# Optimization experiments

Hardware: AMD Instinct MI355X
Metric: run time of the kernel (lower is better)

## Reference

```python
import jax, jax.numpy as jnp
import numpy as np

N_NODES, N_GRAPHS, N_EDGES = 40960, 1024, 163840


def setup_inputs() -> dict:
    key = jax.random.key(0)
    ks = jax.random.split(key, 40)
    w = lambda k, s: jax.random.normal(k, s, jnp.float32) * 0.05
    inp = {
        "x": jax.random.normal(ks[0], (N_NODES, 78), jnp.float32),
        "edge_index": jax.random.randint(ks[1], (2, N_EDGES), 0, N_NODES, jnp.int32),
        "batch": jnp.repeat(jnp.arange(N_GRAPHS, dtype=jnp.int32), N_NODES // N_GRAPHS),
        "target1": jax.random.normal(ks[2], (N_GRAPHS, 750, 20), jnp.float32),
        "target2": jax.random.randint(ks[3], (N_GRAPHS, 750), 0, 26, jnp.int32),
        # GCN layers
        "W1": w(ks[4], (78, 78)), "b1": jnp.zeros((78,), jnp.float32),
        "W2": w(ks[5], (78, 156)), "b2": jnp.zeros((156,), jnp.float32),
        "W3": w(ks[6], (156, 312)), "b3": jnp.zeros((312,), jnp.float32),
        "Wg1": w(ks[7], (312, 1024)), "bg1": jnp.zeros((1024,), jnp.float32),
        "Wg2": w(ks[8], (1024, 128)), "bg2": jnp.zeros((128,), jnp.float32),
        # protein branch
        "emb": w(ks[9], (26, 128)),
        "Wc2": w(ks[10], (32, 750, 8)), "bc2": jnp.zeros((32,), jnp.float32),
        "Wxt2": w(ks[11], (32 * 121, 128)), "bxt2": jnp.zeros((128,), jnp.float32),
        "Wc1": w(ks[12], (32, 750, 8)), "bc1": jnp.zeros((32,), jnp.float32),
        "Wxt1": w(ks[13], (416, 128)), "bxt1": jnp.zeros((128,), jnp.float32),
        # fusion head
        "Wf1": w(ks[14], (384, 1024)), "bf1": jnp.zeros((1024,), jnp.float32),
        "Wf2": w(ks[15], (1024, 512)), "bf2": jnp.zeros((512,), jnp.float32),
        "Wo": w(ks[16], (512, 1)), "bo": jnp.zeros((1,), jnp.float32),
    }
    return inp


def _conv1d(x, w, b):
    # x: [B, C_in, L], w: [C_out, C_in, K] -> [B, C_out, L-K+1]
    y = jax.lax.conv_general_dilated(x, w, (1,), "VALID",
                                     dimension_numbers=("NCH", "OIH", "NCH"))
    return y + b[None, :, None]


def reference(x, edge_index, batch, target1, target2,
              W1, b1, W2, b2, W3, b3, Wg1, bg1, Wg2, bg2,
              emb, Wc2, bc2, Wxt2, bxt2, Wc1, bc1, Wxt1, bxt1,
              Wf1, bf1, Wf2, bf2, Wo, bo):
    N = x.shape[0]
    loop = jnp.arange(N, dtype=edge_index.dtype)
    src = jnp.concatenate([edge_index[0], loop])  # message source j
    dst = jnp.concatenate([edge_index[1], loop])  # aggregation target i
    # symmetric GCN normalization with self-loops (degree from dst, as in PyG)
    deg = jnp.zeros((N,), x.dtype).at[dst].add(1.0)
    dinv = jax.lax.rsqrt(deg)  # deg >= 1 due to self loops
    norm = (dinv[src] * dinv[dst])[:, None]

    def gcn(h, W, b):
        m = (h @ W)[src] * norm
        return jax.ops.segment_sum(m, dst, num_segments=N) + b

    h = jax.nn.relu(gcn(x, W1, b1))
    h = jax.nn.relu(gcn(h, W2, b2))
    h = jax.nn.relu(gcn(h, W3, b3))
    # global max pool per graph
    g = jax.ops.segment_max(h, batch, num_segments=N_GRAPHS)
    g = jax.nn.relu(g @ Wg1 + bg1)
    g = g @ Wg2 + bg2  # dropout is identity at inference

    # protein branch 2: embedding -> conv1d over channels=750
    e = emb[target2]                         # [B, 750, 128]
    xt2 = _conv1d(e, Wc2, bc2)               # [B, 32, 121]
    xt2 = xt2.reshape(-1, 32 * 121) @ Wxt2 + bxt2

    # protein branch 1: raw float features
    xt1 = _conv1d(target1, Wc1, bc1)         # [B, 32, 13]
    xt1 = xt1.reshape(-1, 416) @ Wxt1 + bxt1

    xc = jnp.concatenate([g, xt1, xt2], axis=1)  # [B, 384]
    xc = jax.nn.relu(xc @ Wf1 + bf1)
    xc = jax.nn.relu(xc @ Wf2 + bf2)
    return xc @ Wo + bo
```

## Files before the change

### kernel.cpp

```cpp
#include <hip/hip_runtime.h>
#include <hip/hip_bf16.h>

#define NN 40960
#define NE 163840
#define NB 1024

typedef __attribute__((ext_vector_type(8))) short short8;
typedef __attribute__((ext_vector_type(4))) short short4v;
typedef __attribute__((ext_vector_type(4))) float floatx4;

__device__ inline unsigned short f2bf(float f) {
    union { float f; unsigned u; } v; v.f = f;
    unsigned r = v.u + 0x7fffu + ((v.u >> 16) & 1u);
    return (unsigned short)(r >> 16);
}
__device__ inline float bf2f(unsigned short s) {
    union { unsigned u; float f; } v; v.u = ((unsigned)s) << 16; return v.f;
}
__device__ inline unsigned pack2bf(float lo, float hi) {
    return (unsigned)f2bf(lo) | ((unsigned)f2bf(hi) << 16);
}

static const size_t o_dinv = 0, o_g312 = 40960, o_g1024 = 360448, o_xc = 1409024,
                    o_f1 = 1802240, o_f2 = 2850816, o_b1v = 3375104, o_b2v = 3375232,
                    o_iws = 3375360, o_bufA = 3621124, o_bufB = 16400644;

__global__ __launch_bounds__(256) void k_histprep(
    const int* __restrict__ dst, int* __restrict__ cnt, int* __restrict__ flag,
    const float* __restrict__ W1, const float* __restrict__ W2, const float* __restrict__ W3,
    const float* __restrict__ Wg1, const float* __restrict__ Wg2, const float* __restrict__ Wf1,
    const float* __restrict__ Wf2, unsigned short* __restrict__ Wt,
    const float* __restrict__ Wc2, const float* __restrict__ Wc1,
    float* __restrict__ Wc2r, float* __restrict__ Wc1r,
    const float* __restrict__ Wxt1, float* __restrict__ Btb,
    const float* __restrict__ bc1, const float* __restrict__ bxt1, float* __restrict__ b1v,
    const float* __restrict__ bc2, const float* __restrict__ Wxt2, const float* __restrict__ bxt2,
    float* __restrict__ b2v,
    const float* __restrict__ emb, float* __restrict__ T) {
    __shared__ float el[128];
    int bx = blockIdx.x, tid = threadIdx.x;
    if (bx < 640) {
        int e = bx * 256 + tid;
        if (e < NE) atomicAdd(&cnt[dst[e]], 1);
        return;
    }
    int bp = bx - 640;
    if (bp == 0 && tid == 0) *flag = 0;
    if (bp < 3328) {
        const int cum[8]  = {0, 128, 320, 640, 1664, 1792, 2816, 3328};
        const int KP[7]   = {96, 96, 160, 320, 1024, 384, 1024};
        const int KB[7]   = {78, 78, 156, 312, 1024, 384, 1024};
        const int NNm[7]  = {78, 156, 312, 1024, 128, 1024, 512};
        const size_t OFF[7] = {0, 12288, 30720, 81920, 409600, 540672, 933888};
        int m = 0;
        while (m < 6 && bp >= cum[m + 1]) m++;
        int r = bp - cum[m];
        const float* src = (m == 0) ? W1 : (m == 1) ? W2 : (m == 2) ? W3 : (m == 3) ? Wg1
                         : (m == 4) ? Wg2 : (m == 5) ? Wf1 : Wf2;
        int kp = KP[m], kb = KB[m], nn = NNm[m];
        unsigned short* d = Wt + OFF[m] + (size_t)r * kp;
        for (int k = tid; k < kp; k += 256) {
            float v = (r < nn && k < kb) ? src[(size_t)k * nn + r] : 0.f;
            d[k] = f2bf(v);
        }
    } else if (bp < 4828) {
        int cc = bp - 3328, j = tid;
        const float* W = (cc < 750) ? Wc2 : Wc1;
        float* Wr = (cc < 750) ? Wc2r : Wc1r;
        int c = (cc < 750) ? cc : cc - 750;
        Wr[(size_t)c * 256 + j] = W[(size_t)(j >> 3) * 6000 + c * 8 + (j & 7)];
    } else if (bp < 7388) {
        int idx = (bp - 4828) * 256 + tid;
        int j = idx & 127, ok = (idx >> 7) & 255, t = idx >> 15;
        int o = ok >> 3, k = ok & 7, lpos = t - k;
        float v = (lpos >= 0 && lpos < 13) ? Wxt1[(size_t)(o * 13 + lpos) * 128 + j] : 0.f;
        Btb[(size_t)(t * 256 + ok) * 128 + j] = v;
    } else if (bp < 7452) {
        if (tid >= 128) return;
        int b = bp - 7388, j = tid;
        if (b < 32) {
            const float* p = Wxt1 + (size_t)b * 13 * 128 + j;
            float t = 0.f;
            for (int l = 0; l < 13; l++) t += p[(size_t)l * 128];
            float add = bc1[b] * t + ((b == 0) ? bxt1[j] : 0.f);
            atomicAdd(&b1v[j], add);
        } else {
            int o = b - 32;
            const float* p = Wxt2 + (size_t)o * 121 * 128 + j;
            float t = 0.f;
            for (int l = 0; l < 121; l++) t += p[(size_t)l * 128];
            float add = bc2[o] * t + ((o == 0) ? bxt2[j] : 0.f);
            atomicAdd(&b2v[j], add);
        }
    } else {
        int tb = bp - 7452;
        int v = tb >> 4, op = tb & 15;
        int o = op * 2 + (tid >> 7), j = tid & 127;
        if (tid < 128) el[j] = emb[(size_t)v * 128 + j];
        __syncthreads();
        float acc[8] = {};
        for (int l = 0; l < 121; l++) {
            float w = Wxt2[(size_t)(o * 121 + l) * 128 + j];
#pragma unroll
            for (int k = 0; k < 8; k++) acc[k] += el[l + k] * w;
        }
#pragma unroll
        for (int k = 0; k < 8; k++) T[(size_t)(v * 256 + o * 8 + k) * 128 + j] = acc[k];
    }
}

__global__ __launch_bounds__(1024) void k_scan_all(const int* __restrict__ cnt, int* __restrict__ off,
                                                   int* __restrict__ cur, float* __restrict__ dinv,
                                                   int* __restrict__ blockSum, int* __restrict__ flag) {
    __shared__ int lds[1024];
    __shared__ int bs[40];
    int tid = threadIdx.x, bx = blockIdx.x;
    int i = bx * 1024 + tid;
    int v = cnt[i];
    dinv[i] = rsqrtf((float)v + 1.0f);
    lds[tid] = v;
    __syncthreads();
    for (int s = 1; s < 1024; s <<= 1) {
        int t = (tid >= s) ? lds[tid - s] : 0;
        __syncthreads();
        lds[tid] += t;
        __syncthreads();
    }
    int localExcl = lds[tid] - v;
    if (tid == 1023) {
        atomicExch(&blockSum[bx], lds[1023]);
        __threadfence();
        atomicAdd(flag, 1);
    }
    if (tid == 0) {
        while (atomicAdd(flag, 0) < 40) { }
    }
    __syncthreads();
    if (tid < 40) bs[tid] = atomicAdd(&blockSum[tid], 0);
    __syncthreads();
    int pref = 0;
    for (int j = 0; j < bx; j++) pref += bs[j];
    int o = localExcl + pref;
    off[i] = o;
    cur[i] = o;
    if (i == NN - 1) off[NN] = NE;
}

__global__ __launch_bounds__(64) void k_agg_x(const float* __restrict__ x, const float* __restrict__ dinv,
                                              const int* __restrict__ off, const int* __restrict__ srcs,
                                              unsigned* __restrict__ out) {
    int n = blockIdx.x;
    int f = threadIdx.x;
    if (f >= 48) return;
    if (f >= 39) { out[(size_t)n * 48 + f] = 0; return; }
    float di = dinv[n];
    float2 sv = *(const float2*)&x[(size_t)n * 78 + 2 * f];
    float a0 = sv.x * di * di, a1 = sv.y * di * di;
    int e0 = off[n], e1 = off[n + 1];
    int e = e0;
    for (; e + 4 <= e1; e += 4) {
        int s0 = srcs[e], s1 = srcs[e + 1], s2 = srcs[e + 2], s3 = srcs[e + 3];
        float d0 = dinv[s0] * di, d1 = dinv[s1] * di, d2 = dinv[s2] * di, d3 = dinv[s3] * di;
        float2 v0 = *(const float2*)&x[(size_t)s0 * 78 + 2 * f];
        float2 v1 = *(const float2*)&x[(size_t)s1 * 78 + 2 * f];
        float2 v2 = *(const float2*)&x[(size_t)s2 * 78 + 2 * f];
        float2 v3 = *(const float2*)&x[(size_t)s3 * 78 + 2 * f];
        a0 += v0.x * d0 + v1.x * d1 + v2.x * d2 + v3.x * d3;
        a1 += v0.y * d0 + v1.y * d1 + v2.y * d2 + v3.y * d3;
    }
    for (; e < e1; e++) {
        int s = srcs[e];
        float dd = dinv[s] * di;
        float2 v = *(const float2*)&x[(size_t)s * 78 + 2 * f];
        a0 += v.x * dd; a1 += v.y * dd;
    }
    out[(size_t)n * 48 + f] = pack2bf(a0, a1);
}

__device__ inline void d_agg16_node(int n, int f, const unsigned* __restrict__ h,
                                    const float* __restrict__ dinv, const int* __restrict__ off,
                                    const int* __restrict__ srcs, unsigned* __restrict__ out, int F2) {
    if (f >= F2) return;
    float di = dinv[n];
    unsigned s0v = h[(size_t)n * F2 + f];
    float a0 = bf2f((unsigned short)(s0v & 0xffff)) * di * di;
    float a1 = bf2f((unsigned short)(s0v >> 16)) * di * di;
    int e0 = off[n], e1 = off[n + 1];
    int e = e0;
    for (; e + 4 <= e1; e += 4) {
        int s0 = srcs[e], s1 = srcs[e + 1], s2 = srcs[e + 2], s3 = srcs[e + 3];
        float d0 = dinv[s0] * di, d1 = dinv[s1] * di, d2 = dinv[s2] * di, d3 = dinv[s3] * di;
        unsigned v0 = h[(size_t)s0 * F2 + f];
        unsigned v1 = h[(size_t)s1 * F2 + f];
        unsigned v2 = h[(size_t)s2 * F2 + f];
        unsigned v3 = h[(size_t)s3 * F2 + f];
        a0 += bf2f((unsigned short)(v0 & 0xffff)) * d0 + bf2f((unsigned short)(v1 & 0xffff)) * d1
            + bf2f((unsigned short)(v2 & 0xffff)) * d2 + bf2f((unsigned short)(v3 & 0xffff)) * d3;
        a1 += bf2f((unsigned short)(v0 >> 16)) * d0 + bf2f((unsigned short)(v1 >> 16)) * d1
            + bf2f((unsigned short)(v2 >> 16)) * d2 + bf2f((unsigned short)(v3 >> 16)) * d3;
    }
    for (; e < e1; e++) {
        int s = srcs[e];
        float dd = dinv[s] * di;
        unsigned v = h[(size_t)s * F2 + f];
        a0 += bf2f((unsigned short)(v & 0xffff)) * dd;
        a1 += bf2f((unsigned short)(v >> 16)) * dd;
    }
    out[(size_t)n * F2 + f] = pack2bf(a0, a1);
}

__global__ void k_agg16(const unsigned* __restrict__ h, const float* __restrict__ dinv,
                        const int* __restrict__ off, const int* __restrict__ srcs,
                        unsigned* __restrict__ out, int F2) {
    d_agg16_node(blockIdx.x, threadIdx.x, h, dinv, off, srcs, out, F2);
}

#define LDST 72
template <bool ABF16, bool OUTBF16, bool ATOMIC, bool RELU_OUT>
__global__ __launch_bounds__(256) void gemm_bt(const void* __restrict__ Av, const unsigned short* __restrict__ Bt,
                                               const float* __restrict__ bias, void* __restrict__ Cv,
                                               int Nn, int Npad, int Kpad, int Klim,
                                               int lda, int ldb, int ldc, int ksplit) {
    __shared__ __align__(16) unsigned short As[64 * LDST];
    __shared__ __align__(16) unsigned short Bs[64 * LDST];
    const float* Af = (const float*)Av;
    const unsigned short* A16 = (const unsigned short*)Av;
    float* Cf = (float*)Cv;
    unsigned short* C16 = (unsigned short*)Cv;
    int bn0 = blockIdx.x * 64;
    int bm0 = blockIdx.y * 64;
    int k0 = blockIdx.z * ksplit;
    int kend = k0 + ksplit; if (kend > Kpad) kend = Kpad;
    int tid = threadIdx.x;
    int w = tid >> 6, l = tid & 63, q = l >> 4, r = l & 15;
    int wr = w >> 1, wc = w & 1;

    floatx4 acc[2][2];
#pragma unroll
    for (int i = 0; i < 2; i++)
#pragma unroll
        for (int c = 0; c < 2; c++) acc[i][c] = (floatx4)0.0f;

    int mA = tid >> 2, kcA = (tid & 3) * 8;
    int nB = tid >> 2, kcB = (tid & 3) * 8;
    int gmA = bm0 + mA;
    int gnB = bn0 + nB;

    for (int kt = k0; kt < kend; kt += 32) {
        if (ABF16) {
            *(short8*)&As[mA * LDST + kcA] = *(const short8*)(A16 + (size_t)gmA * lda + kt + kcA);
        } else {
            const float* Ap = Af + (size_t)gmA * lda + kt + kcA;
            float av[8];
            if (kt + kcA + 8 <= Klim) {
#pragma unroll
                for (int j = 0; j < 4; j++) {
                    float2 p = *(const float2*)(Ap + j * 2);
                    av[j * 2] = p.x; av[j * 2 + 1] = p.y;
                }
            } else {
#pragma unroll
                for (int j = 0; j < 8; j++) av[j] = (kt + kcA + j < Klim) ? Ap[j] : 0.f;
            }
            short8 sv;
#pragma unroll
            for (int j = 0; j < 8; j++) sv[j] = (short)f2bf(av[j]);
            *(short8*)&As[mA * LDST + kcA] = sv;
        }
        *(short8*)&Bs[nB * LDST + kcB] = *(const short8*)(Bt + (size_t)gnB * ldb + kt + kcB);
        __syncthreads();
        short8 a0 = *(const short8*)&As[(wr * 32 + r) * LDST + q * 8];
        short8 a1 = *(const short8*)&As[(wr * 32 + 16 + r) * LDST + q * 8];
        short8 b0 = *(const short8*)&Bs[(wc * 32 + r) * LDST + q * 8];
        short8 b1 = *(const short8*)&Bs[(wc * 32 + 16 + r) * LDST + q * 8];
        acc[0][0] = __builtin_amdgcn_mfma_f32_16x16x32_bf16(a0, b0, acc[0][0], 0, 0, 0);
        acc[0][1] = __builtin_amdgcn_mfma_f32_16x16x32_bf16(a0, b1, acc[0][1], 0, 0, 0);
        acc[1][0] = __builtin_amdgcn_mfma_f32_16x16x32_bf16(a1, b0, acc[1][0], 0, 0, 0);
        acc[1][1] = __builtin_amdgcn_mfma_f32_16x16x32_bf16(a1, b1, acc[1][1], 0, 0, 0);
        __syncthreads();
    }

#pragma unroll
    for (int c2 = 0; c2 < 2; c2++) {
        int col = bn0 + wc * 32 + c2 * 16 + r;
        if (col >= Npad) continue;
        bool live = col < Nn;
        float bv = (bias && live) ? bias[col] : 0.f;
#pragma unroll
        for (int i = 0; i < 2; i++) {
#pragma unroll
            for (int v = 0; v < 4; v++) {
                int row = bm0 + wr * 32 + i * 16 + q * 4 + v;
                float val = live ? (acc[i][c2][v] + bv) : 0.f;
                if (RELU_OUT) val = fmaxf(val, 0.f);
                if (OUTBF16) {
                    C16[(size_t)row * ldc + col] = live ? f2bf(val) : (unsigned short)0;
                } else if (live) {
                    if (ATOMIC) atomicAdd(&Cf[(size_t)row * ldc + col], val);
                    else Cf[(size_t)row * ldc + col] = val;
                }
            }
        }
    }
}

__global__ __launch_bounds__(256) void k_fbi(
    const int* __restrict__ ei, int* __restrict__ cur, int* __restrict__ srcOut,
    const float* __restrict__ Wc2r, const float* __restrict__ T,
    const float* __restrict__ Wc1r, const float* __restrict__ Btb,
    unsigned short* __restrict__ U16, unsigned short* __restrict__ Vt16,
    float* __restrict__ xc, float* __restrict__ f2,
    const float* __restrict__ bg2, const float* __restrict__ b1v, const float* __restrict__ bf2) {
    __shared__ __align__(16) unsigned short As[64 * LDST];
    __shared__ __align__(16) unsigned short Bs[64 * LDST];
    int bx = blockIdx.x, tid = threadIdx.x;
    if (bx < 640) {
        int e = bx * 256 + tid;
        if (e >= NE) return;
        int s = ei[e], d = ei[NE + e];
        int pos = atomicAdd(&cur[d], 1);
        srcOut[pos] = s;
        return;
    }
    if (bx >= 1744) {
        int b = bx - 1744;
        for (int t = tid; t < 768; t += 256) {
            if (t < 128) xc[(size_t)b * 384 + t] = bg2[t];
            else if (t < 256) xc[(size_t)b * 384 + t] = b1v[t - 128];
            else f2[(size_t)b * 512 + t - 256] = bf2[t - 256];
        }
        return;
    }
    int v = bx - 640;
    int gx = v & 1, gy = (v >> 1) % 12, gz = (v >> 1) / 12;
    const int M = 750, Nn = 128, K = 256;
    bool om1 = gz < 26;
    const float* A = om1 ? Wc2r : Wc1r;
    const float* Bm = om1 ? (T + (size_t)gz * 32768) : (Btb + (size_t)(gz - 26) * 32768);
    unsigned short* C16 = om1 ? (U16 + (size_t)gz * 128) : Vt16;
    int ldc = om1 ? 3328 : 15360;
    int zz = gz - 26;
    int bn0 = gx * 64;
    int bm0 = gy * 64;
    int w = tid >> 6, l = tid & 63, q = l >> 4, r = l & 15;
    int wr = w >> 1, wc = w & 1;

    floatx4 acc[2][2];
#pragma unroll
    for (int i = 0; i < 2; i++)
#pragma unroll
        for (int c = 0; c < 2; c++) acc[i][c] = (floatx4)0.0f;

    int mA = tid >> 2, kcA = (tid & 3) * 8;
    int nB = tid >> 2, kcB = (tid & 3) * 8;
    int gmA = bm0 + mA;
    int gnB = bn0 + nB;

    for (int kt = 0; kt < K; kt += 32) {
        {
            float av[8];
            const float* Ap = A + (size_t)gmA * K + kt + kcA;
            if (gmA < M) {
#pragma unroll
                for (int j = 0; j < 4; j++) {
                    float2 p = *(const float2*)(Ap + j * 2);
                    av[j * 2] = p.x; av[j * 2 + 1] = p.y;
                }
            } else {
#pragma unroll
                for (int j = 0; j < 8; j++) av[j] = 0.f;
            }
            short8 sv;
#pragma unroll
            for (int j = 0; j < 8; j++) sv[j] = (short)f2bf(av[j]);
            *(short8*)&As[mA * LDST + kcA] = sv;
        }
        {
            short8 sv;
#pragma unroll
            for (int j = 0; j < 8; j++) {
                int gk = kt + kcB + j;
                float vv = (gnB < Nn) ? Bm[(size_t)gk * Nn + gnB] : 0.f;
                sv[j] = (short)f2bf(vv);
            }
            *(short8*)&Bs[nB * LDST + kcB] = sv;
        }
        __syncthreads();
        short8 a0 = *(const short8*)&As[(wr * 32 + r) * LDST + q * 8];
        short8 a1 = *(const short8*)&As[(wr * 32 + 16 + r) * LDST + q * 8];
        short8 b0 = *(const short8*)&Bs[(wc * 32 + r) * LDST + q * 8];
        short8 b1 = *(const short8*)&Bs[(wc * 32 + 16 + r) * LDST + q * 8];
        acc[0][0] = __builtin_amdgcn_mfma_f32_16x16x32_bf16(a0, b0, acc[0][0], 0, 0, 0);
        acc[0][1] = __builtin_amdgcn_mfma_f32_16x16x32_bf16(a0, b1, acc[0][1], 0, 0, 0);
        acc[1][0] = __builtin_amdgcn_mfma_f32_16x16x32_bf16(a1, b0, acc[1][0], 0, 0, 0);
        acc[1][1] = __builtin_amdgcn_mfma_f32_16x16x32_bf16(a1, b1, acc[1][1], 0, 0, 0);
        __syncthreads();
    }

#pragma unroll
    for (int c = 0; c < 2; c++) {
        int col = bn0 + wc * 32 + c * 16 + r;
        if (col >= Nn) continue;
#pragma unroll
        for (int i = 0; i < 2; i++) {
#pragma unroll
            for (int vv = 0; vv < 4; vv++) {
                int row = bm0 + wr * 32 + i * 16 + q * 4 + vv;
                if (row >= M) continue;
                if (om1) C16[(size_t)row * ldc + col] = f2bf(acc[i][c][vv]);
                else C16[(size_t)col * ldc + row * 20 + zz] = f2bf(acc[i][c][vv]);
            }
        }
    }
}

#define T1LD 40
#define T1S  48
#define T1K  320
__global__ __launch_bounds__(256) void k_t1_l1(
    const float* __restrict__ t1A, const unsigned short* __restrict__ Bt, float* __restrict__ P,
    const unsigned short* __restrict__ A16, const unsigned short* __restrict__ W1t,
    const float* __restrict__ bias, unsigned short* __restrict__ C16) {
    __shared__ __align__(16) unsigned char smem[30720];
    int bx = blockIdx.x, tid = threadIdx.x;
    if (bx < 768) {
        unsigned short* AsS = (unsigned short*)smem;
        unsigned short* BsS = (unsigned short*)smem + 5120;
        const int Klim = 15000;
        int mt = bx & 15, ks = bx >> 4;
        int bm0 = mt * 64;
        int k0 = ks * T1K;
        int w = tid >> 6, l = tid & 63, q = l >> 4, r = l & 15;
        int wr = w >> 1, wc = w & 1;

        floatx4 acc[2][4];
#pragma unroll
        for (int i = 0; i < 2; i++)
#pragma unroll
            for (int c = 0; c < 4; c++) acc[i][c] = (floatx4)0.0f;

        int ra = tid >> 3, ca = (tid & 7) * 4;
        int rb = tid >> 2, cb = (tid & 3) * 8;
        const float* Ap0 = t1A + (size_t)(bm0 + ra) * Klim + ca;
        const float* Ap1 = t1A + (size_t)(bm0 + ra + 32) * Klim + ca;
        const unsigned short* Bp0 = Bt + (size_t)rb * 15360 + cb;
        const unsigned short* Bp1 = Bt + (size_t)(rb + 64) * 15360 + cb;

        float4 aA0, aA1, aB0, aB1;
        short8 bA0, bA1, bB0, bB1;

        auto loadT = [&](int kt, float4& x0, float4& x1, short8& y0, short8& y1) {
            int c = kt + ca;
            if (c < Klim) {
                x0 = *(const float4*)(Ap0 + kt);
                x1 = *(const float4*)(Ap1 + kt);
            } else {
                x0 = make_float4(0.f, 0.f, 0.f, 0.f);
                x1 = make_float4(0.f, 0.f, 0.f, 0.f);
            }
            y0 = *(const short8*)(Bp0 + kt);
            y1 = *(const short8*)(Bp1 + kt);
        };
        auto stageW = [&](int buf, const float4& x0, const float4& x1, const short8& y0, const short8& y1) {
            short4v s0, s1;
            s0[0] = (short)f2bf(x0.x); s0[1] = (short)f2bf(x0.y); s0[2] = (short)f2bf(x0.z); s0[3] = (short)f2bf(x0.w);
            s1[0] = (short)f2bf(x1.x); s1[1] = (short)f2bf(x1.y); s1[2] = (short)f2bf(x1.z); s1[3] = (short)f2bf(x1.w);
            *(short4v*)&AsS[buf * 2560 + ra * T1LD + ca] = s0;
            *(short4v*)&AsS[buf * 2560 + (ra + 32) * T1LD + ca] = s1;
            *(short8*)&BsS[buf * 5120 + rb * T1LD + cb] = y0;
            *(short8*)&BsS[buf * 5120 + (rb + 64) * T1LD + cb] = y1;
        };
        auto compute = [&](int buf) {
            short8 a0 = *(const short8*)&AsS[buf * 2560 + (wr * 32 + r) * T1LD + q * 8];
            short8 a1 = *(const short8*)&AsS[buf * 2560 + (wr * 32 + 16 + r) * T1LD + q * 8];
            short8 b0 = *(const short8*)&BsS[buf * 5120 + (wc * 64 + r) * T1LD + q * 8];
            short8 b1 = *(const short8*)&BsS[buf * 5120 + (wc * 64 + 16 + r) * T1LD + q * 8];
            short8 b2 = *(const short8*)&BsS[buf * 5120 + (wc * 64 + 32 + r) * T1LD + q * 8];
            short8 b3 = *(const short8*)&BsS[buf * 5120 + (wc * 64 + 48 + r) * T1LD + q * 8];
            acc[0][0] = __builtin_amdgcn_mfma_f32_16x16x32_bf16(a0, b0, acc[0][0], 0, 0, 0);
            acc[0][1] = __builtin_amdgcn_mfma_f32_16x16x32_bf16(a0, b1, acc[0][1], 0, 0, 0);
            acc[0][2] = __builtin_amdgcn_mfma_f32_16x16x32_bf16(a0, b2, acc[0][2], 0, 0, 0);
            acc[0][3] = __builtin_amdgcn_mfma_f32_16x16x32_bf16(a0, b3, acc[0][3], 0, 0, 0);
            acc[1][0] = __builtin_amdgcn_mfma_f32_16x16x32_bf16(a1, b0, acc[1][0], 0, 0, 0);
            acc[1][1] = __builtin_amdgcn_mfma_f32_16x16x32_bf16(a1, b1, acc[1][1], 0, 0, 0);
            acc[1][2] = __builtin_amdgcn_mfma_f32_16x16x32_bf16(a1, b2, acc[1][2], 0, 0, 0);
            acc[1][3] = __builtin_amdgcn_mfma_f32_16x16x32_bf16(a1, b3, acc[1][3], 0, 0, 0);
        };

        loadT(k0, aA0, aA1, bA0, bA1);
        loadT(k0 + 32, aB0, aB1, bB0, bB1);
#pragma unroll
        for (int it = 0; it < T1K / 32; it += 2) {
            stageW(0, aA0, aA1, bA0, bA1);
            if (it + 2 < T1K / 32) loadT(k0 + (it + 2) * 32, aA0, aA1, bA0, bA1);
            asm volatile("s_waitcnt lgkmcnt(0)" ::: "memory");
            __builtin_amdgcn_s_barrier();
            asm volatile("" ::: "memory");
            compute(0);
            stageW(1, aB0, aB1, bB0, bB1);
            if (it + 3 < T1K / 32) loadT(k0 + (it + 3) * 32, aB0, aB1, bB0, bB1);
            asm volatile("s_waitcnt lgkmcnt(0)" ::: "memory");
            __builtin_amdgcn_s_barrier();
            asm volatile("" ::: "memory");
            compute(1);
        }

        float* Pp = P + (size_t)ks * (1024 * 128) + (size_t)bm0 * 128;
#pragma unroll
        for (int c = 0; c < 4; c++) {
            int col = wc * 64 + c * 16 + r;
#pragma unroll
            for (int i = 0; i < 2; i++) {
#pragma unroll
                for (int v = 0; v < 4; v++) {
                    int row = wr * 32 + i * 16 + q * 4 + v;
                    Pp[(size_t)row * 128 + col] = acc[i][c][v];
                }
            }
        }
    } else {
        unsigned short* As = (unsigned short*)smem;
        unsigned short* Bs = (unsigned short*)smem + 4608;
        int v = bx - 768;
        int bn0 = (v & 1) * 64;
        int bm0 = (v >> 1) * 64;
        int w = tid >> 6, l = tid & 63, q = l >> 4, r = l & 15;
        int wr = w >> 1, wc = w & 1;

        floatx4 acc[2][2];
#pragma unroll
        for (int i = 0; i < 2; i++)
#pragma unroll
            for (int c = 0; c < 2; c++) acc[i][c] = (floatx4)0.0f;

        int mA = tid >> 2, kcA = (tid & 3) * 8;
        int gmA = bm0 + mA;
        int gnB = bn0 + mA;

        for (int kt = 0; kt < 96; kt += 32) {
            *(short8*)&As[mA * LDST + kcA] = *(const short8*)(A16 + (size_t)gmA * 96 + kt + kcA);
            *(short8*)&Bs[mA * LDST + kcA] = *(const short8*)(W1t + (size_t)gnB * 96 + kt + kcA);
            __syncthreads();
            short8 a0 = *(const short8*)&As[(wr * 32 + r) * LDST + q * 8];
            short8 a1 = *(const short8*)&As[(wr * 32 + 16 + r) * LDST + q * 8];
            short8 b0 = *(const short8*)&Bs[(wc * 32 + r) * LDST + q * 8];
            short8 b1 = *(const short8*)&Bs[(wc * 32 + 16 + r) * LDST + q * 8];
            acc[0][0] = __builtin_amdgcn_mfma_f32_16x16x32_bf16(a0, b0, acc[0][0], 0, 0, 0);
            acc[0][1] = __builtin_amdgcn_mfma_f32_16x16x32_bf16(a0, b1, acc[0][1], 0, 0, 0);
            acc[1][0] = __builtin_amdgcn_mfma_f32_16x16x32_bf16(a1, b0, acc[1][0], 0, 0, 0);
            acc[1][1] = __builtin_amdgcn_mfma_f32_16x16x32_bf16(a1, b1, acc[1][1], 0, 0, 0);
            __syncthreads();
        }

#pragma unroll
        for (int c2 = 0; c2 < 2; c2++) {
            int col = bn0 + wc * 32 + c2 * 16 + r;
            if (col >= 96) continue;
            bool live = col < 78;
            float bv = live ? bias[col] : 0.f;
#pragma unroll
            for (int i = 0; i < 2; i++) {
#pragma unroll
                for (int vv = 0; vv < 4; vv++) {
                    int row = bm0 + wr * 32 + i * 16 + q * 4 + vv;
                    float val = live ? fmaxf(acc[i][c2][vv] + bv, 0.f) : 0.f;
                    C16[(size_t)row * 96 + col] = live ? f2bf(val) : (unsigned short)0;
                }
            }
        }
    }
}

__global__ __launch_bounds__(128) void k_agg16_ug(
    const unsigned* __restrict__ h, const float* __restrict__ dinv, const int* __restrict__ off,
    const int* __restrict__ srcs, unsigned* __restrict__ outb,
    const int* __restrict__ t2, const unsigned short* __restrict__ U,
    const float* __restrict__ b2v, float* __restrict__ xc) {
    __shared__ int offs[752];
    __shared__ float red[8][128];
    int bx = blockIdx.x, tid = threadIdx.x;
    if (bx < NB) {
        int b = bx;
        int rg = tid >> 4, lane = tid & 15;
        const int* t2b = t2 + (size_t)b * 750;
        for (int i = tid; i < 750; i += 128) offs[i] = i * 3328 + t2b[i] * 128;
        __syncthreads();
        float a[8] = {};
#pragma unroll 4
        for (int i = rg; i < 750; i += 8) {
            short8 v = *(const short8*)&U[(size_t)offs[i] + lane * 8];
#pragma unroll
            for (int c = 0; c < 8; c++) a[c] += bf2f((unsigned short)v[c]);
        }
#pragma unroll
        for (int c = 0; c < 8; c++) red[rg][lane * 8 + c] = a[c];
        __syncthreads();
        float s = b2v[tid];
#pragma unroll
        for (int g = 0; g < 8; g++) s += red[g][tid];
        xc[(size_t)b * 384 + 256 + tid] = s;
    } else {
        d_agg16_node(bx - NB, tid, h, dinv, off, srcs, outb, 80);
    }
}

__global__ void k_segmax_red(const unsigned short* __restrict__ h, unsigned short* __restrict__ g,
                             const float* __restrict__ P, float* __restrict__ xc) {
    int bx = blockIdx.x, tid = threadIdx.x;
    if (bx < NB) {
        if (tid < 128) {
            int row = bx, j = tid;
            const float* p = P + (size_t)row * 128 + j;
            float s = 0.f;
#pragma unroll
            for (int ks = 0; ks < T1S; ks++) s += p[(size_t)ks * (1024 * 128)];
            xc[(size_t)row * 384 + 128 + j] += s;
        }
    } else {
        int gr = bx - NB, f = tid;
        if (f >= 320) return;
        if (f >= 312) { g[(size_t)gr * 320 + f] = 0; return; }
        float m = 0.0f;
        const unsigned short* base = h + (size_t)gr * 40 * 312 + f;
        for (int i = 0; i < 40; i++) m = fmaxf(m, bf2f(base[(size_t)i * 312]));
        g[(size_t)gr * 320 + f] = f2bf(m);
    }
}

__global__ __launch_bounds__(64) void k_final(const float* __restrict__ f2, const float* __restrict__ Wo,
                                              const float* __restrict__ bo, float* __restrict__ out) {
    int b = blockIdx.x, lane = threadIdx.x;
    float s = 0.f;
    for (int j = lane; j < 512; j += 64) s += fmaxf(f2[(size_t)b * 512 + j], 0.f) * Wo[j];
    for (int off = 32; off; off >>= 1) s += __shfl_down(s, off);
    if (lane == 0) out[b] = s + bo[0];
}

extern "C" void kernel_launch(void* const* d_in, const int* in_sizes, int n_in,
                              void* d_out, int out_size, void* d_ws, size_t ws_size,
                              hipStream_t stream) {
    const float* x    = (const float*)d_in[0];
    const int*   ei   = (const int*)d_in[1];
    const float* t1   = (const float*)d_in[3];
    const int*   t2   = (const int*)d_in[4];
    const float* W1   = (const float*)d_in[5];
    const float* b1   = (const float*)d_in[6];
    const float* W2   = (const float*)d_in[7];
    const float* b2   = (const float*)d_in[8];
    const float* W3   = (const float*)d_in[9];
    const float* b3   = (const float*)d_in[10];
    const float* Wg1  = (const float*)d_in[11];
    const float* bg1  = (const float*)d_in[12];
    const float* Wg2  = (const float*)d_in[13];
    const float* bg2  = (const float*)d_in[14];
    const float* emb  = (const float*)d_in[15];
    const float* Wc2  = (const float*)d_in[16];
    const float* bc2  = (const float*)d_in[17];
    const float* Wxt2 = (const float*)d_in[18];
    const float* bxt2 = (const float*)d_in[19];
    const float* Wc1  = (const float*)d_in[20];
    const float* bc1  = (const float*)d_in[21];
    const float* Wxt1 = (const float*)d_in[22];
    const float* bxt1 = (const float*)d_in[23];
    const float* Wf1  = (const float*)d_in[24];
    const float* bf1  = (const float*)d_in[25];
    const float* Wf2  = (const float*)d_in[26];
    const float* bf2  = (const float*)d_in[27];
    const float* Wo   = (const float*)d_in[28];
    const float* bo   = (const float*)d_in[29];
    float* out = (float*)d_out;

    float* ws = (float*)d_ws;
    float* dinv  = ws + o_dinv;
    unsigned short* g312b = (unsigned short*)(ws + o_g312);
    unsigned short* g1024b = (unsigned short*)(ws + o_g1024);
    float* xc    = ws + o_xc;
    unsigned short* f1b = (unsigned short*)(ws + o_f1);
    float* f2    = ws + o_f2;
    float* b1v   = ws + o_b1v;
    float* b2v   = ws + o_b2v;
    int* csrOff  = (int*)(ws + o_iws);
    int* csrCur  = csrOff + (NN + 1);
    int* csrSrc  = csrCur + NN;
    int* blockSum = (int*)(ws + o_f1 + 600000);
    int* scanFlag = blockSum + 63;
    float* bufA  = ws + o_bufA;
    float* bufB  = ws + o_bufB;
    float* T    = bufA;
    unsigned short* U16  = (unsigned short*)(bufA + 851968);
    unsigned short* Vt16 = (unsigned short*)(bufA + 2200000);
    unsigned short* Wt   = (unsigned short*)(bufA + 3200000);
    float* Wc2r = bufA + 4000000;
    float* Wc1r = bufA + 4200000;
    float* Btb  = bufA + 4400000;
    float* Pt1  = bufA + 6000000;
    unsigned* aggb = (unsigned*)bufB;
    unsigned short* h16 = (unsigned short*)(bufB + 5500000);

    unsigned short* W1t  = Wt + 0;
    unsigned short* W2t  = Wt + 12288;
    unsigned short* W3t  = Wt + 30720;
    unsigned short* Wg1t = Wt + 81920;
    unsigned short* Wg2t = Wt + 409600;
    unsigned short* Wf1t = Wt + 540672;
    unsigned short* Wf2t = Wt + 933888;

    hipMemsetAsync(Vt16, 0, (size_t)128 * 15360 * 2, stream);
    hipMemsetAsync(b1v, 0, 256 * sizeof(float), stream);
    hipMemsetAsync(csrCur, 0, NN * sizeof(int), stream);

    k_histprep<<<8508, 256, 0, stream>>>(ei + NE, csrCur, scanFlag,
                                         W1, W2, W3, Wg1, Wg2, Wf1, Wf2, Wt,
                                         Wc2, Wc1, Wc2r, Wc1r,
                                         Wxt1, Btb, bc1, bxt1, b1v,
                                         bc2, Wxt2, bxt2, b2v, emb, T);

    k_scan_all<<<40, 1024, 0, stream>>>(csrCur, csrOff, csrCur, dinv, blockSum, scanFlag);

    k_fbi<<<2768, 256, 0, stream>>>(ei, csrCur, csrSrc, Wc2r, T, Wc1r, Btb, U16, Vt16,
                                    xc, f2, bg2, b1v, bf2);

    k_agg_x<<<NN, 64, 0, stream>>>(x, dinv, csrOff, csrSrc, aggb);

    k_t1_l1<<<2048, 256, 0, stream>>>(t1, Vt16, Pt1, (const unsigned short*)aggb, W1t, b1, h16);

    k_agg16<<<NN, 64, 0, stream>>>((unsigned*)h16, dinv, csrOff, csrSrc, aggb, 48);
    gemm_bt<true, true, false, true><<<dim3(3, 640, 1), 256, 0, stream>>>(
        aggb, W2t, b2, h16, 156, 160, 96, 96, 96, 96, 160, 96);
    k_agg16_ug<<<NB + NN, 128, 0, stream>>>((unsigned*)h16, dinv, csrOff, csrSrc, aggb,
                                            t2, U16, b2v, xc);
    gemm_bt<true, true, false, true><<<dim3(5, 640, 1), 256, 0, stream>>>(
        aggb, W3t, b3, h16, 312, 312, 160, 160, 160, 160, 312, 160);
    k_segmax_red<<<2 * NB, 320, 0, stream>>>(h16, g312b, Pt1, xc);
    gemm_bt<true, true, false, true><<<dim3(16, 16, 1), 256, 0, stream>>>(
        g312b, Wg1t, bg1, g1024b, 1024, 1024, 320, 320, 320, 320, 1024, 320);

    gemm_bt<true, false, true, false><<<dim3(2, 16, 8), 256, 0, stream>>>(
        g1024b, Wg2t, nullptr, xc + 0, 128, 128, 1024, 1024, 1024, 1024, 384, 128);

    gemm_bt<false, true, false, true><<<dim3(16, 16, 1), 256, 0, stream>>>(
        xc, Wf1t, bf1, f1b, 1024, 1024, 384, 384, 384, 384, 1024, 384);
    gemm_bt<true, false, true, false><<<dim3(8, 16, 4), 256, 0, stream>>>(
        f1b, Wf2t, nullptr, f2, 512, 512, 1024, 1024, 1024, 1024, 512, 256);
    k_final<<<NB, 64, 0, stream>>>(f2, Wo, bo, out);
}
```

Baseline: 419.9 us.

## Split target1 conv split-K work across GCN layer-1 and layer-2 GEMM launches

The fused kernel that pairs the target1 conv split-K GEMM with a GCN linear layer now takes a K-slice base, a slice count and layer parameters. The 768 conv blocks are split into two halves of 384. One half runs with the layer-1 GEMM and the other replaces the standalone layer-2 gemm_bt launch. The aim is to balance work across launches and fill idle CUs in the small GCN GEMMs. The layer-2 GEMM now uses this kernel's simpler unpipelined tile loop instead of gemm_bt, which could be slower for that layer.

```diff
diff --git a/kernel.cpp b/kernel.cpp
--- a/kernel.cpp
+++ b/kernel.cpp
@@ -417,17 +417,19 @@
 #define T1LD 40
 #define T1S  48
 #define T1K  320
-__global__ __launch_bounds__(256) void k_t1_l1(
+__global__ __launch_bounds__(256) void k_t1_gcn(
     const float* __restrict__ t1A, const unsigned short* __restrict__ Bt, float* __restrict__ P,
-    const unsigned short* __restrict__ A16, const unsigned short* __restrict__ W1t,
-    const float* __restrict__ bias, unsigned short* __restrict__ C16) {
+    int ksBase, int nT1,
+    const unsigned short* __restrict__ A16, const unsigned short* __restrict__ Wg,
+    const float* __restrict__ bias, unsigned short* __restrict__ C16,
+    int Nn, int Npad, int ldc, int gridX) {
     __shared__ __align__(16) unsigned char smem[30720];
     int bx = blockIdx.x, tid = threadIdx.x;
-    if (bx < 768) {
+    if (bx < nT1) {
         unsigned short* AsS = (unsigned short*)smem;
         unsigned short* BsS = (unsigned short*)smem + 5120;
         const int Klim = 15000;
-        int mt = bx & 15, ks = bx >> 4;
+        int mt = bx & 15, ks = ksBase + (bx >> 4);
         int bm0 = mt * 64;
         int k0 = ks * T1K;
         int w = tid >> 6, l = tid & 63, q = l >> 4, r = l & 15;
@@ -521,9 +523,9 @@
     } else {
         unsigned short* As = (unsigned short*)smem;
         unsigned short* Bs = (unsigned short*)smem + 4608;
-        int v = bx - 768;
-        int bn0 = (v & 1) * 64;
-        int bm0 = (v >> 1) * 64;
+        int v = bx - nT1;
+        int bn0 = (v % gridX) * 64;
+        int bm0 = (v / gridX) * 64;
         int w = tid >> 6, l = tid & 63, q = l >> 4, r = l & 15;
         int wr = w >> 1, wc = w & 1;
 
@@ -539,7 +541,7 @@
 
         for (int kt = 0; kt < 96; kt += 32) {
             *(short8*)&As[mA * LDST + kcA] = *(const short8*)(A16 + (size_t)gmA * 96 + kt + kcA);
-            *(short8*)&Bs[mA * LDST + kcA] = *(const short8*)(W1t + (size_t)gnB * 96 + kt + kcA);
+            *(short8*)&Bs[mA * LDST + kcA] = *(const short8*)(Wg + (size_t)gnB * 96 + kt + kcA);
             __syncthreads();
             short8 a0 = *(const short8*)&As[(wr * 32 + r) * LDST + q * 8];
             short8 a1 = *(const short8*)&As[(wr * 32 + 16 + r) * LDST + q * 8];
@@ -555,8 +557,8 @@
 #pragma unroll
         for (int c2 = 0; c2 < 2; c2++) {
             int col = bn0 + wc * 32 + c2 * 16 + r;
-            if (col >= 96) continue;
-            bool live = col < 78;
+            if (col >= Npad) continue;
+            bool live = col < Nn;
             float bv = live ? bias[col] : 0.f;
 #pragma unroll
             for (int i = 0; i < 2; i++) {
@@ -564,7 +566,7 @@
                 for (int vv = 0; vv < 4; vv++) {
                     int row = bm0 + wr * 32 + i * 16 + q * 4 + vv;
                     float val = live ? fmaxf(acc[i][c2][vv] + bv, 0.f) : 0.f;
-                    C16[(size_t)row * 96 + col] = live ? f2bf(val) : (unsigned short)0;
+                    C16[(size_t)row * ldc + col] = live ? f2bf(val) : (unsigned short)0;
                 }
             }
         }
@@ -722,11 +724,16 @@
 
     k_agg_x<<<NN, 64, 0, stream>>>(x, dinv, csrOff, csrSrc, aggb);
 
-    k_t1_l1<<<2048, 256, 0, stream>>>(t1, Vt16, Pt1, (const unsigned short*)aggb, W1t, b1, h16);
+    k_t1_gcn<<<384 + 1280, 256, 0, stream>>>(t1, Vt16, Pt1, 0, 384,
+                                             (const unsigned short*)aggb, W1t, b1, h16,
+                                             78, 96, 96, 2);
 
     k_agg16<<<NN, 64, 0, stream>>>((unsigned*)h16, dinv, csrOff, csrSrc, aggb, 48);
-    gemm_bt<true, true, false, true><<<dim3(3, 640, 1), 256, 0, stream>>>(
-        aggb, W2t, b2, h16, 156, 160, 96, 96, 96, 96, 160, 96);
+
+    k_t1_gcn<<<384 + 1920, 256, 0, stream>>>(t1, Vt16, Pt1, 24, 384,
+                                             (const unsigned short*)aggb, W2t, b2, h16,
+                                             156, 160, 160, 3);
+
     k_agg16_ug<<<NB + NN, 128, 0, stream>>>((unsigned*)h16, dinv, csrOff, csrSrc, aggb,
                                             t2, U16, b2v, xc);
     gemm_bt<true, true, false, true><<<dim3(5, 640, 1), 256, 0, stream>>>(
```

After: 424.6 us. About the same (+1.1%).
